# Kernel tuning notes

Hardware: AMD Instinct MI355X
Metric: run time of the kernel (lower is better)

The kernel has to match this reference:

```python
import jax, jax.numpy as jnp
import numpy as np

N_NODES = 50000
N_EDGES = 800000
IN_CH = 128
HEADS = 4
OUT_CH = 32
NEG_SLOPE = 0.2


def setup_inputs() -> dict:
    key = jax.random.key(0)
    ks = jax.random.split(key, 7)
    x = jax.random.normal(ks[0], (N_NODES, IN_CH), dtype=jnp.float32)
    src = jax.random.randint(ks[1], (N_EDGES,), 0, N_NODES, dtype=jnp.int32)
    dst = jax.random.randint(ks[2], (N_EDGES,), 0, N_NODES, dtype=jnp.int32)
    W = jax.random.normal(ks[3], (IN_CH, HEADS * OUT_CH), dtype=jnp.float32) * (1.0 / np.sqrt(IN_CH))
    attn_l = jax.random.normal(ks[4], (HEADS, OUT_CH), dtype=jnp.float32) * 0.1
    attn_r = jax.random.normal(ks[5], (HEADS, OUT_CH), dtype=jnp.float32) * 0.1
    bias = jnp.zeros((HEADS * OUT_CH,), dtype=jnp.float32)
    return {"x": x, "src": src, "dst": dst, "W": W, "attn_l": attn_l, "attn_r": attn_r, "bias": bias}


def reference(x, src, dst, W, attn_l, attn_r, bias):
    n = x.shape[0]
    # Linear projection -> per-head features [N, H, D]
    feat = (x @ W).reshape(n, HEADS, OUT_CH)
    # Node-level attention terms [N, H]
    el = jnp.einsum('nhd,hd->nh', feat, attn_l)
    er = jnp.einsum('nhd,hd->nh', feat, attn_r)
    # Edge attention logits [E, H]
    e = jax.nn.leaky_relu(el[src] + er[dst], negative_slope=NEG_SLOPE)
    # Segment softmax over incoming edges of each dst node
    m = jax.ops.segment_max(e, dst, num_segments=n)          # [N, H]
    m = jnp.where(jnp.isfinite(m), m, 0.0)
    ex = jnp.exp(e - m[dst])                                  # [E, H]
    s = jax.ops.segment_sum(ex, dst, num_segments=n)          # [N, H]
    alpha = ex / s[dst]                                       # [E, H]
    # Weighted message aggregation: scatter-add to dst [N, H, D]
    msg = feat[src] * alpha[:, :, None]
    out = jax.ops.segment_sum(msg, dst, num_segments=n)
    out = out + bias.reshape(HEADS, OUT_CH)
    # agg='mean' over heads -> [N, D]
    return out.mean(axis=1)
```

## Files before the change

### kernel.cpp

```cpp
#include <hip/hip_runtime.h>

#define IN_CH 128
#define NEG_SLOPE 0.2f
#define MAXDEG 64

#define GTILE 64
#define EPB 1024

typedef short bf16x8 __attribute__((ext_vector_type(8)));
typedef float floatx4 __attribute__((ext_vector_type(4)));

static __device__ __forceinline__ unsigned short f2bf(float f) {
    union { float f; unsigned int u; } a; a.f = f;
    unsigned int u = a.u;
    u += 0x7fffu + ((u >> 16) & 1u);
    return (unsigned short)(u >> 16);
}

__global__ void k_prep(const float* __restrict__ W,
                       const float* __restrict__ attn_l,
                       const float* __restrict__ attn_r,
                       unsigned short* __restrict__ Wtb2,
                       int* __restrict__ cnt, int N) {
    int i = blockIdx.x * 256 + threadIdx.x;
    if (i < N) cnt[(size_t)i << 4] = 0;
    if (i < 128 * 128) {
        int n = i >> 7, k = i & 127;
        Wtb2[(size_t)n * 128 + k] = f2bf(W[(size_t)k * 128 + n]);
    }
    if (i < 1024) {
        int row = i >> 7;
        int k = i & 127;
        int h = row & 3;
        const float* av = (row < 4) ? attn_l : attn_r;
        const float* wp = W + (size_t)k * 128 + h * 32;
        float s = 0.f;
#pragma unroll
        for (int d = 0; d < 32; ++d) s += wp[d] * av[h * 32 + d];
        Wtb2[(size_t)(128 + row) * 128 + k] = f2bf(s);
    }
    if (i >= 1024 && i < 2048) {
        int row = 136 + ((i - 1024) >> 7);
        Wtb2[(size_t)row * 128 + (i & 127)] = 0;
    }
}

__global__ __launch_bounds__(256, 4) void k_fused(const float* __restrict__ x,
                                                  const unsigned short* __restrict__ Wtb2,
                                                  unsigned short* __restrict__ featb,
                                                  float* __restrict__ el,
                                                  float* __restrict__ er, int N,
                                                  const int* __restrict__ src,
                                                  const int* __restrict__ dst,
                                                  int* __restrict__ cnt,
                                                  unsigned short* __restrict__ esrc_pad, int E,
                                                  int GB, int RB) {
    __shared__ __align__(16) unsigned short Al[16 * 136];
    int b = blockIdx.x;
    int M2 = 2 * (GB < RB ? GB : RB);
    bool is_edge;
    int part;
    if (b < M2) { is_edge = (b & 1); part = b >> 1; }
    else        { is_edge = (RB > GB); part = (M2 >> 1) + (b - M2); }

    if (is_edge) {
        int e0 = part * EPB + threadIdx.x * 4;
        if (e0 < E) {
            int4 s4 = *(const int4*)(src + e0);
            int4 d4 = *(const int4*)(dst + e0);
            int r0 = atomicAdd(&cnt[(size_t)d4.x << 4], 1);
            int r1 = atomicAdd(&cnt[(size_t)d4.y << 4], 1);
            int r2 = atomicAdd(&cnt[(size_t)d4.z << 4], 1);
            int r3 = atomicAdd(&cnt[(size_t)d4.w << 4], 1);
            if (r0 < MAXDEG) esrc_pad[(size_t)d4.x * MAXDEG + r0] = (unsigned short)s4.x;
            if (r1 < MAXDEG) esrc_pad[(size_t)d4.y * MAXDEG + r1] = (unsigned short)s4.y;
            if (r2 < MAXDEG) esrc_pad[(size_t)d4.z * MAXDEG + r2] = (unsigned short)s4.z;
            if (r3 < MAXDEG) esrc_pad[(size_t)d4.w * MAXDEG + r3] = (unsigned short)s4.w;
        }
        return;
    }

    int base = part * GTILE;
    int ntile = (N - base + 15) >> 4; if (ntile > 4) ntile = 4;

    int wave = threadIdx.x >> 6;
    int lane = threadIdx.x & 63;
    int l15 = lane & 15;
    int quad = lane >> 4;
    int r0 = wave * 16 + l15;
    int r1 = 64 + wave * 16 + l15;
    int r2 = 128 + l15;

    bf16x8 b0f[4], b1f[4], b2f[4];
    {
        const unsigned short* bp0 = Wtb2 + (size_t)r0 * 128 + quad * 8;
        const unsigned short* bp1 = Wtb2 + (size_t)r1 * 128 + quad * 8;
        const unsigned short* bp2 = Wtb2 + (size_t)r2 * 128 + quad * 8;
#pragma unroll
        for (int kk = 0; kk < 4; ++kk) {
            b0f[kk] = *(const bf16x8*)(bp0 + kk * 32);
            b1f[kk] = *(const bf16x8*)(bp1 + kk * 32);
            b2f[kk] = *(const bf16x8*)(bp2 + kk * 32);
        }
    }

    float4 xr[2];
    {
        const float4* xt = (const float4*)(x + (size_t)base * 128);
#pragma unroll
        for (int i = 0; i < 2; ++i) {
            float4 u = xt[threadIdx.x + 256 * i];
            int f = (threadIdx.x + 256 * i) * 4;
            int row = f >> 7, col = f & 127;
            ushort4 pk;
            pk.x = f2bf(u.x); pk.y = f2bf(u.y); pk.z = f2bf(u.z); pk.w = f2bf(u.w);
            *(ushort4*)(Al + row * 136 + col) = pk;
        }
        if (ntile > 1) {
            const float4* xt1 = (const float4*)(x + (size_t)(base + 16) * 128);
#pragma unroll
            for (int i = 0; i < 2; ++i) xr[i] = xt1[threadIdx.x + 256 * i];
        }
    }
    __syncthreads();

    for (int t = 0; t < ntile; ++t) {
        int m0 = base + t * 16;
        const unsigned short* ap = Al + l15 * 136 + quad * 8;
        floatx4 acc0 = {0.f, 0.f, 0.f, 0.f};
        floatx4 acc1 = {0.f, 0.f, 0.f, 0.f};
        floatx4 acc2 = {0.f, 0.f, 0.f, 0.f};
#pragma unroll
        for (int kk = 0; kk < 4; ++kk) {
            bf16x8 a = *(const bf16x8*)(ap + kk * 32);
            acc0 = __builtin_amdgcn_mfma_f32_16x16x32_bf16(a, b0f[kk], acc0, 0, 0, 0);
            acc1 = __builtin_amdgcn_mfma_f32_16x16x32_bf16(a, b1f[kk], acc1, 0, 0, 0);
            if (wave == 0)
                acc2 = __builtin_amdgcn_mfma_f32_16x16x32_bf16(a, b2f[kk], acc2, 0, 0, 0);
        }
#pragma unroll
        for (int r = 0; r < 4; ++r) {
            size_t row = (size_t)(m0 + quad * 4 + r) * 128;
            featb[row + r0] = f2bf(acc0[r]);
            featb[row + r1] = f2bf(acc1[r]);
        }
        if (wave == 0) {
#pragma unroll
            for (int r = 0; r < 4; ++r) {
                int m = m0 + quad * 4 + r;
                if (l15 < 4)      el[(size_t)m * 4 + l15]       = acc2[r];
                else if (l15 < 8) er[(size_t)m * 4 + (l15 - 4)] = acc2[r];
            }
        }
        __syncthreads();
        if (t + 1 < ntile) {
#pragma unroll
            for (int i = 0; i < 2; ++i) {
                int f = (threadIdx.x + 256 * i) * 4;
                int row = f >> 7, col = f & 127;
                ushort4 pk;
                pk.x = f2bf(xr[i].x); pk.y = f2bf(xr[i].y);
                pk.z = f2bf(xr[i].z); pk.w = f2bf(xr[i].w);
                *(ushort4*)(Al + row * 136 + col) = pk;
            }
            if (t + 2 < ntile) {
                const float4* xt2 = (const float4*)(x + (size_t)(base + (t + 2) * 16) * 128);
#pragma unroll
                for (int i = 0; i < 2; ++i) xr[i] = xt2[threadIdx.x + 256 * i];
            }
        }
        __syncthreads();
    }
}

__global__ __launch_bounds__(256) void k_node(const int* __restrict__ cnt,
                                              const unsigned short* __restrict__ esrc_pad,
                                              const float* __restrict__ el,
                                              const float* __restrict__ er,
                                              const unsigned short* __restrict__ featb,
                                              const float* __restrict__ bias,
                                              float* __restrict__ out, int N) {
    int n = blockIdx.x * 4 + (threadIdx.x >> 6);
    if (n >= N) return;
    int lane = threadIdx.x & 63;
    int g = lane >> 4;
    int r = lane & 15;
    int h = r >> 2;
    int deg = cnt[(size_t)n << 4];
    if (deg > MAXDEG) deg = MAXDEG;
    const unsigned short* ep = esrc_pad + (size_t)n * MAXDEG;
    int epw = ((const int*)ep)[lane & 31];
    float erh = er[(size_t)n * 4 + h];
    float s = 0.f;
    float a0 = 0.f, a1 = 0.f, a2 = 0.f, a3 = 0.f;
    float a4 = 0.f, a5 = 0.f, a6 = 0.f, a7 = 0.f;

    int w0 = __shfl(epw, (g >> 1) & 31);
    int sn0 = (g < deg) ? ((w0 >> ((g & 1) << 4)) & 0xffff) : 0;
    int j1 = g + 4;
    int w1 = __shfl(epw, (j1 >> 1) & 31);
    int sn1 = (j1 < deg) ? ((w1 >> ((j1 & 1) << 4)) & 0xffff) : 0;
    float el0 = el[(size_t)sn0 * 4 + h];
    uint4 q0 = *(const uint4*)(featb + (size_t)sn0 * 128 + r * 8);
    float el1 = el[(size_t)sn1 * 4 + h];
    uint4 q1 = *(const uint4*)(featb + (size_t)sn1 * 128 + r * 8);

    for (int t4 = 0; t4 < deg; t4 += 4) {
        int j = t4 + g;
        int jp = j + 8;
        int w2 = __shfl(epw, (jp >> 1) & 31);
        int sn2 = (jp < deg) ? ((w2 >> ((jp & 1) << 4)) & 0xffff) : 0;
        float el2 = el[(size_t)sn2 * 4 + h];
        uint4 q2 = *(const uint4*)(featb + (size_t)sn2 * 128 + r * 8);
        float t = el0 + erh;
        float e = __expf(t > 0.f ? t : NEG_SLOPE * t);
        e = (j < deg) ? e : 0.f;
        s += e;
        a0 += e * __uint_as_float(q0.x << 16);
        a1 += e * __uint_as_float(q0.x & 0xffff0000u);
        a2 += e * __uint_as_float(q0.y << 16);
        a3 += e * __uint_as_float(q0.y & 0xffff0000u);
        a4 += e * __uint_as_float(q0.z << 16);
        a5 += e * __uint_as_float(q0.z & 0xffff0000u);
        a6 += e * __uint_as_float(q0.w << 16);
        a7 += e * __uint_as_float(q0.w & 0xffff0000u);
        el0 = el1; q0 = q1;
        el1 = el2; q1 = q2;
    }

    s  += __shfl_xor(s, 16);  s  += __shfl_xor(s, 32);
    a0 += __shfl_xor(a0, 16); a0 += __shfl_xor(a0, 32);
    a1 += __shfl_xor(a1, 16); a1 += __shfl_xor(a1, 32);
    a2 += __shfl_xor(a2, 16); a2 += __shfl_xor(a2, 32);
    a3 += __shfl_xor(a3, 16); a3 += __shfl_xor(a3, 32);
    a4 += __shfl_xor(a4, 16); a4 += __shfl_xor(a4, 32);
    a5 += __shfl_xor(a5, 16); a5 += __shfl_xor(a5, 32);
    a6 += __shfl_xor(a6, 16); a6 += __shfl_xor(a6, 32);
    a7 += __shfl_xor(a7, 16); a7 += __shfl_xor(a7, 32);
    float inv = (deg > 0) ? 0.25f / s : 0.f;
    a0 *= inv; a1 *= inv; a2 *= inv; a3 *= inv;
    a4 *= inv; a5 *= inv; a6 *= inv; a7 *= inv;
    a0 += __shfl_xor(a0, 4); a0 += __shfl_xor(a0, 8);
    a1 += __shfl_xor(a1, 4); a1 += __shfl_xor(a1, 8);
    a2 += __shfl_xor(a2, 4); a2 += __shfl_xor(a2, 8);
    a3 += __shfl_xor(a3, 4); a3 += __shfl_xor(a3, 8);
    a4 += __shfl_xor(a4, 4); a4 += __shfl_xor(a4, 8);
    a5 += __shfl_xor(a5, 4); a5 += __shfl_xor(a5, 8);
    a6 += __shfl_xor(a6, 4); a6 += __shfl_xor(a6, 8);
    a7 += __shfl_xor(a7, 4); a7 += __shfl_xor(a7, 8);
    if (lane < 4) {
        int dd = lane * 8;
        float4 o0, o1;
        o0.x = a0 + 0.25f * (bias[dd + 0] + bias[32 + dd + 0] + bias[64 + dd + 0] + bias[96 + dd + 0]);
        o0.y = a1 + 0.25f * (bias[dd + 1] + bias[32 + dd + 1] + bias[64 + dd + 1] + bias[96 + dd + 1]);
        o0.z = a2 + 0.25f * (bias[dd + 2] + bias[32 + dd + 2] + bias[64 + dd + 2] + bias[96 + dd + 2]);
        o0.w = a3 + 0.25f * (bias[dd + 3] + bias[32 + dd + 3] + bias[64 + dd + 3] + bias[96 + dd + 3]);
        o1.x = a4 + 0.25f * (bias[dd + 4] + bias[32 + dd + 4] + bias[64 + dd + 4] + bias[96 + dd + 4]);
        o1.y = a5 + 0.25f * (bias[dd + 5] + bias[32 + dd + 5] + bias[64 + dd + 5] + bias[96 + dd + 5]);
        o1.z = a6 + 0.25f * (bias[dd + 6] + bias[32 + dd + 6] + bias[64 + dd + 6] + bias[96 + dd + 6]);
        o1.w = a7 + 0.25f * (bias[dd + 7] + bias[32 + dd + 7] + bias[64 + dd + 7] + bias[96 + dd + 7]);
        *(float4*)(out + (size_t)n * 32 + dd) = o0;
        *(float4*)(out + (size_t)n * 32 + dd + 4) = o1;
    }
}

extern "C" void kernel_launch(void* const* d_in, const int* in_sizes, int n_in,
                              void* d_out, int out_size, void* d_ws, size_t ws_size,
                              hipStream_t stream) {
    const float* x      = (const float*)d_in[0];
    const int*   src    = (const int*)d_in[1];
    const int*   dst    = (const int*)d_in[2];
    const float* W      = (const float*)d_in[3];
    const float* attn_l = (const float*)d_in[4];
    const float* attn_r = (const float*)d_in[5];
    const float* bias   = (const float*)d_in[6];
    float* out = (float*)d_out;

    int N = in_sizes[0] / IN_CH;
    int E = in_sizes[1];
    int GB = (N + GTILE - 1) / GTILE;
    int RB = (E + EPB - 1) / EPB;

    char* w = (char*)d_ws;
    unsigned short* featb = (unsigned short*)w; w += (size_t)N * 128 * 2;
    unsigned short* Wtb2  = (unsigned short*)w; w += 144 * 128 * 2;
    float* el       = (float*)w;  w += (size_t)N * 4 * 4;
    float* er       = (float*)w;  w += (size_t)N * 4 * 4;
    int*   cnt      = (int*)w;    w += (size_t)N * 16 * 4;
    unsigned short* esrc_pad = (unsigned short*)w; w += (size_t)N * MAXDEG * 2;

    k_prep<<<(N + 255) / 256, 256, 0, stream>>>(W, attn_l, attn_r, Wtb2, cnt, N);
    k_fused<<<GB + RB, 256, 0, stream>>>(x, Wtb2, featb, el, er, N,
                                         src, dst, cnt, esrc_pad, E, GB, RB);
    k_node<<<(N + 3) / 4, 256, 0, stream>>>(cnt, esrc_pad, el, er, featb, bias, out, N);
}
```

Measured before the change: 153.7 us.

## Replace global atomic CSR build with two-pass shared-memory bucketed adjacency build

Edge blocks no longer do global atomics per destination node. Each block instead bins its edges into 256-node buckets with shared-memory atomics and writes packed (local dst, src) pairs into fixed-capacity per-block segments. A new k_bucket kernel then gathers each bucket's segments, builds the padded adjacency in shared memory, and writes it and the degree counts out with coalesced stores. This removes scattered global atomics and the per-node count reset, at the cost of an extra kernel launch and a capacity cap of 32 edges per bucket per block, which could drop edges if a block's edges cluster.

```diff
diff --git a/kernel.cpp b/kernel.cpp
--- a/kernel.cpp
+++ b/kernel.cpp
@@ -6,6 +6,9 @@
 
 #define GTILE 64
 #define EPB 1024
+#define NPB 256
+#define NBUCK 196
+#define CAP 32
 
 typedef short bf16x8 __attribute__((ext_vector_type(8)));
 typedef float floatx4 __attribute__((ext_vector_type(4)));
@@ -20,10 +23,8 @@
 __global__ void k_prep(const float* __restrict__ W,
                        const float* __restrict__ attn_l,
                        const float* __restrict__ attn_r,
-                       unsigned short* __restrict__ Wtb2,
-                       int* __restrict__ cnt, int N) {
+                       unsigned short* __restrict__ Wtb2) {
     int i = blockIdx.x * 256 + threadIdx.x;
-    if (i < N) cnt[(size_t)i << 4] = 0;
     if (i < 128 * 128) {
         int n = i >> 7, k = i & 127;
         Wtb2[(size_t)n * 128 + k] = f2bf(W[(size_t)k * 128 + n]);
@@ -52,10 +53,11 @@
                                                   float* __restrict__ er, int N,
                                                   const int* __restrict__ src,
                                                   const int* __restrict__ dst,
-                                                  int* __restrict__ cnt,
-                                                  unsigned short* __restrict__ esrc_pad, int E,
+                                                  unsigned int* __restrict__ gseg,
+                                                  unsigned char* __restrict__ cnt8, int E,
                                                   int GB, int RB) {
     __shared__ __align__(16) unsigned short Al[16 * 136];
+    __shared__ int lcnt[NBUCK];
     int b = blockIdx.x;
     int M2 = 2 * (GB < RB ? GB : RB);
     bool is_edge;
@@ -64,18 +66,32 @@
     else        { is_edge = (RB > GB); part = (M2 >> 1) + (b - M2); }
 
     if (is_edge) {
+        for (int i = threadIdx.x; i < NBUCK; i += 256) lcnt[i] = 0;
+        __syncthreads();
         int e0 = part * EPB + threadIdx.x * 4;
+        unsigned int pk0 = 0, pk1 = 0, pk2 = 0, pk3 = 0;
+        int bk0 = -1, bk1 = -1, bk2 = -1, bk3 = -1;
+        int r0 = 0, r1 = 0, r2 = 0, r3 = 0;
         if (e0 < E) {
             int4 s4 = *(const int4*)(src + e0);
             int4 d4 = *(const int4*)(dst + e0);
-            int r0 = atomicAdd(&cnt[(size_t)d4.x << 4], 1);
-            int r1 = atomicAdd(&cnt[(size_t)d4.y << 4], 1);
-            int r2 = atomicAdd(&cnt[(size_t)d4.z << 4], 1);
-            int r3 = atomicAdd(&cnt[(size_t)d4.w << 4], 1);
-            if (r0 < MAXDEG) esrc_pad[(size_t)d4.x * MAXDEG + r0] = (unsigned short)s4.x;
-            if (r1 < MAXDEG) esrc_pad[(size_t)d4.y * MAXDEG + r1] = (unsigned short)s4.y;
-            if (r2 < MAXDEG) esrc_pad[(size_t)d4.z * MAXDEG + r2] = (unsigned short)s4.z;
-            if (r3 < MAXDEG) esrc_pad[(size_t)d4.w * MAXDEG + r3] = (unsigned short)s4.w;
+            bk0 = d4.x >> 8; pk0 = ((unsigned int)(d4.x & 255) << 16) | (unsigned int)s4.x;
+            bk1 = d4.y >> 8; pk1 = ((unsigned int)(d4.y & 255) << 16) | (unsigned int)s4.y;
+            bk2 = d4.z >> 8; pk2 = ((unsigned int)(d4.z & 255) << 16) | (unsigned int)s4.z;
+            bk3 = d4.w >> 8; pk3 = ((unsigned int)(d4.w & 255) << 16) | (unsigned int)s4.w;
+            r0 = atomicAdd(&lcnt[bk0], 1);
+            r1 = atomicAdd(&lcnt[bk1], 1);
+            r2 = atomicAdd(&lcnt[bk2], 1);
+            r3 = atomicAdd(&lcnt[bk3], 1);
+            if (r0 < CAP) gseg[((size_t)bk0 * RB + part) * CAP + r0] = pk0;
+            if (r1 < CAP) gseg[((size_t)bk1 * RB + part) * CAP + r1] = pk1;
+            if (r2 < CAP) gseg[((size_t)bk2 * RB + part) * CAP + r2] = pk2;
+            if (r3 < CAP) gseg[((size_t)bk3 * RB + part) * CAP + r3] = pk3;
+        }
+        __syncthreads();
+        for (int i = threadIdx.x; i < NBUCK; i += 256) {
+            int c = lcnt[i]; if (c > CAP) c = CAP;
+            cnt8[(size_t)part * NBUCK + i] = (unsigned char)c;
         }
         return;
     }
@@ -87,15 +103,15 @@
     int lane = threadIdx.x & 63;
     int l15 = lane & 15;
     int quad = lane >> 4;
-    int r0 = wave * 16 + l15;
-    int r1 = 64 + wave * 16 + l15;
-    int r2 = 128 + l15;
+    int rr0 = wave * 16 + l15;
+    int rr1 = 64 + wave * 16 + l15;
+    int rr2 = 128 + l15;
 
     bf16x8 b0f[4], b1f[4], b2f[4];
     {
-        const unsigned short* bp0 = Wtb2 + (size_t)r0 * 128 + quad * 8;
-        const unsigned short* bp1 = Wtb2 + (size_t)r1 * 128 + quad * 8;
-        const unsigned short* bp2 = Wtb2 + (size_t)r2 * 128 + quad * 8;
+        const unsigned short* bp0 = Wtb2 + (size_t)rr0 * 128 + quad * 8;
+        const unsigned short* bp1 = Wtb2 + (size_t)rr1 * 128 + quad * 8;
+        const unsigned short* bp2 = Wtb2 + (size_t)rr2 * 128 + quad * 8;
 #pragma unroll
         for (int kk = 0; kk < 4; ++kk) {
             b0f[kk] = *(const bf16x8*)(bp0 + kk * 32);
@@ -141,8 +157,8 @@
 #pragma unroll
         for (int r = 0; r < 4; ++r) {
             size_t row = (size_t)(m0 + quad * 4 + r) * 128;
-            featb[row + r0] = f2bf(acc0[r]);
-            featb[row + r1] = f2bf(acc1[r]);
+            featb[row + rr0] = f2bf(acc0[r]);
+            featb[row + rr1] = f2bf(acc1[r]);
         }
         if (wave == 0) {
 #pragma unroll
@@ -170,6 +186,43 @@
             }
         }
         __syncthreads();
+    }
+}
+
+__global__ __launch_bounds__(512) void k_bucket(const unsigned int* __restrict__ gseg,
+                                                const unsigned char* __restrict__ cnt8,
+                                                unsigned short* __restrict__ esrc_pad,
+                                                int* __restrict__ cnt, int N, int RB) {
+    __shared__ unsigned short adj[NPB * MAXDEG];
+    __shared__ int ndeg[NPB];
+    __shared__ unsigned char c8[800];
+    int bkt = blockIdx.x;
+    for (int i = threadIdx.x; i < NPB; i += 512) ndeg[i] = 0;
+    for (int i = threadIdx.x; i < RB; i += 512) c8[i] = cnt8[(size_t)i * NBUCK + bkt];
+    __syncthreads();
+    const unsigned int* seg = gseg + (size_t)bkt * RB * CAP;
+    const int total = RB * CAP;
+    for (int s = threadIdx.x; s < total; s += 512) {
+        int blk = s >> 5;
+        int slot = s & 31;
+        if (slot < (int)c8[blk]) {
+            unsigned int ed = seg[s];
+            int ln = (int)(ed >> 16) & (NPB - 1);
+            int r = atomicAdd(&ndeg[ln], 1);
+            if (r < MAXDEG) adj[ln * MAXDEG + r] = (unsigned short)(ed & 0xffffu);
+        }
+    }
+    __syncthreads();
+    int n0 = bkt * NPB;
+    int nvalid = N - n0; if (nvalid > NPB) nvalid = NPB;
+    if (nvalid <= 0) return;
+    int words = nvalid * (MAXDEG / 8);
+    const uint4* asrc = (const uint4*)adj;
+    uint4* adst = (uint4*)(esrc_pad + (size_t)n0 * MAXDEG);
+    for (int i = threadIdx.x; i < words; i += 512) adst[i] = asrc[i];
+    for (int i = threadIdx.x; i < nvalid; i += 512) {
+        int d = ndeg[i]; if (d > MAXDEG) d = MAXDEG;
+        cnt[n0 + i] = d;
     }
 }
 
@@ -186,7 +239,7 @@
     int g = lane >> 4;
     int r = lane & 15;
     int h = r >> 2;
-    int deg = cnt[(size_t)n << 4];
+    int deg = cnt[n];
     if (deg > MAXDEG) deg = MAXDEG;
     const unsigned short* ep = esrc_pad + (size_t)n * MAXDEG;
     int epw = ((const int*)ep)[lane & 31];
@@ -286,11 +339,14 @@
     unsigned short* Wtb2  = (unsigned short*)w; w += 144 * 128 * 2;
     float* el       = (float*)w;  w += (size_t)N * 4 * 4;
     float* er       = (float*)w;  w += (size_t)N * 4 * 4;
-    int*   cnt      = (int*)w;    w += (size_t)N * 16 * 4;
+    int*   cnt      = (int*)w;    w += (size_t)N * 4;
     unsigned short* esrc_pad = (unsigned short*)w; w += (size_t)N * MAXDEG * 2;
-
-    k_prep<<<(N + 255) / 256, 256, 0, stream>>>(W, attn_l, attn_r, Wtb2, cnt, N);
+    unsigned int*   gseg = (unsigned int*)w; w += (size_t)NBUCK * RB * CAP * 4;
+    unsigned char*  cnt8 = (unsigned char*)w; w += (size_t)RB * NBUCK;
+
+    k_prep<<<64, 256, 0, stream>>>(W, attn_l, attn_r, Wtb2);
     k_fused<<<GB + RB, 256, 0, stream>>>(x, Wtb2, featb, el, er, N,
-                                         src, dst, cnt, esrc_pad, E, GB, RB);
+                                         src, dst, gseg, cnt8, E, GB, RB);
+    k_bucket<<<NBUCK, 512, 0, stream>>>(gseg, cnt8, esrc_pad, cnt, N, RB);
     k_node<<<(N + 3) / 4, 256, 0, stream>>>(cnt, esrc_pad, el, er, featb, bias, out, N);
 }
```

After: 155.8 us. No clear change (+1.3%).
